# Kernel tuning notes

Hardware: AMD Instinct MI355X
Metric: run time of the kernel (lower is better)

## Reference

```python
import jax, jax.numpy as jnp
import numpy as np

N_NODES, N_EDGES = 50000, 800000
N_IN, E_IN, N_OUT, E_OUT = 64, 32, 64, 32


def _xavier(key, fan_in, fan_out):
    std = (2.0 / (fan_in + fan_out)) ** 0.5
    return jax.random.normal(key, (fan_in, fan_out), dtype=jnp.float32) * std


def setup_inputs() -> dict:
    key = jax.random.key(0)
    ks = jax.random.split(key, 10)
    return {
        "feat": jax.random.normal(ks[0], (N_NODES, N_IN), dtype=jnp.float32),
        "edge_feat": jax.random.normal(ks[1], (N_EDGES, E_IN), dtype=jnp.float32),
        "w_msg": _xavier(ks[2], N_IN + E_IN, N_OUT),
        "b_msg": jnp.zeros((N_OUT,), dtype=jnp.float32),
        "w_node": _xavier(ks[3], N_IN + N_OUT, N_OUT),
        "b_node": jnp.zeros((N_OUT,), dtype=jnp.float32),
        "w_edge": _xavier(ks[4], N_IN + N_OUT + E_IN, E_OUT),
        "b_edge": jnp.zeros((E_OUT,), dtype=jnp.float32),
        "src_idx": jax.random.randint(ks[5], (N_EDGES,), 0, N_NODES, dtype=jnp.int32),
        "dst_idx": jax.random.randint(ks[6], (N_EDGES,), 0, N_NODES, dtype=jnp.int32),
    }


def reference(feat, edge_feat, w_msg, b_msg, w_node, b_node, w_edge, b_edge, src_idx, dst_idx):
    n_nodes = feat.shape[0]
    # --- message: gather src + edge, linear, tanh --- [E, n_out]
    src_h = feat[src_idx]
    m = jnp.tanh(jnp.concatenate([src_h, edge_feat], axis=1) @ w_msg + b_msg)
    # --- scatter-mean into destination nodes --- [N, n_out]
    sums = jax.ops.segment_sum(m, dst_idx, num_segments=n_nodes)
    cnt = jax.ops.segment_sum(jnp.ones((m.shape[0], 1), m.dtype), dst_idx, num_segments=n_nodes)
    neigh = sums / jnp.maximum(cnt, 1.0)
    # --- node update: cat([neigh, h]) -> linear -> tanh (dropout = identity in eval) ---
    h = jnp.tanh(jnp.concatenate([neigh, feat], axis=1) @ w_node + b_node)
    # --- edge update: cat([src h, dst neigh(updated), edge h]) -> linear -> tanh ---
    e = jnp.tanh(jnp.concatenate([src_h, h[dst_idx], edge_feat], axis=1) @ w_edge + b_edge)
    return h, e
```

## Files before the change

kernel.cpp:

```cpp
#include <hip/hip_runtime.h>

#define NNODES 50000
#define NEDGES 800000
#define NPAD   50176
#define NTILE_E (NEDGES / 16)
#define NTILE_N (NNODES / 16)

typedef __attribute__((ext_vector_type(8))) short bf16x8;
typedef __attribute__((ext_vector_type(4))) float f32x4;

union ABu { bf16x8 v; uint4 u; };

__device__ __forceinline__ float fast_tanh(float x) {
    float e = __expf(2.0f * x);
    return 1.0f - 2.0f * __builtin_amdgcn_rcpf(e + 1.0f);
}

__device__ __forceinline__ unsigned pk_rne(float x, float y) {
    unsigned a = __float_as_uint(x), b = __float_as_uint(y);
    a = (a + 0x7fffu + ((a >> 16) & 1u)) >> 16;
    b = (b + 0x7fffu + ((b >> 16) & 1u)) >> 16;
    return a | (b << 16);
}
__device__ __forceinline__ unsigned pk_tr(float a, float b) {
    return __builtin_amdgcn_perm(__float_as_uint(b), __float_as_uint(a), 0x07060302);
}
__device__ __forceinline__ float bf16_lo(unsigned u) { return __uint_as_float(u << 16); }
__device__ __forceinline__ float bf16_hi(unsigned u) { return __uint_as_float(u & 0xffff0000u); }

__device__ __forceinline__ ABu make_afrag(const float* p) {
    float4 a = ((const float4*)p)[0];
    float4 b = ((const float4*)p)[1];
    ABu r;
    r.u.x = pk_tr(a.x, a.y); r.u.y = pk_tr(a.z, a.w);
    r.u.z = pk_tr(b.x, b.y); r.u.w = pk_tr(b.z, b.w);
    return r;
}

template <int LDW>
__device__ __forceinline__ ABu make_bfrag(const float* wp) {
    ABu r;
    r.u.x = pk_rne(wp[0 * LDW], wp[1 * LDW]);
    r.u.y = pk_rne(wp[2 * LDW], wp[3 * LDW]);
    r.u.z = pk_rne(wp[4 * LDW], wp[5 * LDW]);
    r.u.w = pk_rne(wp[6 * LDW], wp[7 * LDW]);
    return r;
}

#define MFMA(a, b, c) __builtin_amdgcn_mfma_f32_16x16x32_bf16((a).v, (b).v, (c), 0, 0, 0)

__global__ __launch_bounds__(256) void hist_kernel(const int* __restrict__ dst_idx,
                                                   int* __restrict__ cnt) {
    const int t = blockIdx.x * 256 + threadIdx.x;
    const int base = t * 4;
    if (base + 4 <= NEDGES) {
        int4 d = *(const int4*)(dst_idx + base);
        atomicAdd(&cnt[d.x], 1);
        atomicAdd(&cnt[d.y], 1);
        atomicAdd(&cnt[d.z], 1);
        atomicAdd(&cnt[d.w], 1);
    } else {
        for (int i = base; i < NEDGES; ++i) atomicAdd(&cnt[dst_idx[i]], 1);
    }
}

__global__ __launch_bounds__(256) void msg_kernel(
    const float* __restrict__ feat, const float* __restrict__ edge_feat,
    const float* __restrict__ w_msg, const float* __restrict__ b_msg,
    const int* __restrict__ src_idx, const int* __restrict__ dst_idx,
    unsigned* __restrict__ m_out, int* __restrict__ off) {
    __shared__ __align__(16) float wl[96 * 64];
    for (int i = threadIdx.x; i < 96 * 64; i += 256) wl[i] = w_msg[i];
    __syncthreads();

    const int lane = threadIdx.x & 63, wave = threadIdx.x >> 6;
    const int col = lane & 15, quad = lane >> 4;

    ABu bf[3][4];
#pragma unroll
    for (int kc = 0; kc < 3; ++kc)
#pragma unroll
        for (int nt = 0; nt < 4; ++nt)
            bf[kc][nt] = make_bfrag<64>(&wl[(kc * 32 + quad * 8) * 64 + nt * 16 + col]);

    float bias[4];
#pragma unroll
    for (int nt = 0; nt < 4; ++nt) bias[nt] = b_msg[nt * 16 + col];

    const int nw = gridDim.x << 2;
    for (int t = (blockIdx.x << 2) + wave; t < NTILE_E; t += nw) {
        const int e0 = t << 4;
        const int e = e0 + col;
        const int src = src_idx[e];
        int pos = 0;
        if (quad == 0) pos = atomicAdd(&off[dst_idx[e]], 1);

        ABu a0 = make_afrag(feat + (size_t)src * 64 + quad * 8);
        ABu a1 = make_afrag(feat + (size_t)src * 64 + 32 + quad * 8);
        ABu a2 = make_afrag(edge_feat + (size_t)e * 32 + quad * 8);

        f32x4 acc[4];
#pragma unroll
        for (int nt = 0; nt < 4; ++nt)
            acc[nt] = (f32x4){bias[nt], bias[nt], bias[nt], bias[nt]};
#pragma unroll
        for (int nt = 0; nt < 4; ++nt) {
            acc[nt] = MFMA(a0, bf[0][nt], acc[nt]);
            acc[nt] = MFMA(a1, bf[1][nt], acc[nt]);
            acc[nt] = MFMA(a2, bf[2][nt], acc[nt]);
        }
#pragma unroll
        for (int i = 0; i < 4; ++i) {
            const int row = __shfl(pos, (quad << 2) + i);
            uint2 o;
            o.x = pk_rne(fast_tanh(acc[0][i]), fast_tanh(acc[1][i]));
            o.y = pk_rne(fast_tanh(acc[2][i]), fast_tanh(acc[3][i]));
            *(uint2*)(m_out + (size_t)row * 32 + (col << 1)) = o;
        }
    }
}

__global__ __launch_bounds__(256) void scan1(const int* __restrict__ cnt,
                                             int* __restrict__ off,
                                             int* __restrict__ btot) {
    __shared__ int s[256];
    const int tid = threadIdx.x;
    const int g = blockIdx.x * 256 + tid;
    const int own = cnt[g];
    s[tid] = own;
    __syncthreads();
    for (int o = 1; o < 256; o <<= 1) {
        int v = (tid >= o) ? s[tid - o] : 0;
        __syncthreads();
        s[tid] += v;
        __syncthreads();
    }
    off[g] = s[tid] - own;
    if (tid == 255) btot[blockIdx.x] = s[255];
}

__global__ __launch_bounds__(256) void scan2(int* __restrict__ btot) {
    __shared__ int s[256];
    const int tid = threadIdx.x;
    const int own = btot[tid];
    s[tid] = own;
    __syncthreads();
    for (int o = 1; o < 256; o <<= 1) {
        int v = (tid >= o) ? s[tid - o] : 0;
        __syncthreads();
        s[tid] += v;
        __syncthreads();
    }
    btot[tid] = s[tid] - own;
}

__global__ __launch_bounds__(256) void scan3(int* __restrict__ off,
                                             const int* __restrict__ btot) {
    const int g = blockIdx.x * 256 + threadIdx.x;
    off[g] += btot[blockIdx.x];
}

__global__ __launch_bounds__(256) void gather_kernel(
    const unsigned* __restrict__ m,
    const int* __restrict__ off , const int* __restrict__ cnt,
    float* __restrict__ neigh) {
    const int wave = threadIdx.x >> 6;
    const int lane = threadIdx.x & 63;
    const int n = blockIdx.x * 4 + wave;
    if (n >= NNODES) return;
    const int c = cnt[n];
    const int o = off[n] - c;
    const int q = lane & 15;
    const int g = lane >> 4;

    float a0 = 0.f, a1 = 0.f, a2 = 0.f, a3 = 0.f;
    for (int r = g; r < c; r += 4) {
        const uint2 u = *(const uint2*)(m + (size_t)(o + r) * 32 + (q << 1));
        a0 += bf16_lo(u.x);
        a1 += bf16_hi(u.x);
        a2 += bf16_lo(u.y);
        a3 += bf16_hi(u.y);
    }
    a0 += __shfl_xor(a0, 16); a1 += __shfl_xor(a1, 16);
    a2 += __shfl_xor(a2, 16); a3 += __shfl_xor(a3, 16);
    a0 += __shfl_xor(a0, 32); a1 += __shfl_xor(a1, 32);
    a2 += __shfl_xor(a2, 32); a3 += __shfl_xor(a3, 32);
    if (g == 0) {
        const float inv = __builtin_amdgcn_rcpf((float)max(c, 1));
        float4 o4 = {a0 * inv, a1 * inv, a2 * inv, a3 * inv};
        ((float4*)(neigh + (size_t)n * 64))[q] = o4;
    }
}

__device__ __forceinline__ int mapk(int ks) {
    return ks < 64 ? ((ks >> 2) + ((ks >> 1) & 1) * 32 + (ks & 1) * 16) : ks;
}

__global__ __launch_bounds__(256) void node_update(
    const float* __restrict__ feat,
    const float* __restrict__ w_node, const float* __restrict__ b_node,
    float* __restrict__ h) {
    __shared__ __align__(16) float wl[128 * 64];
    for (int i = threadIdx.x; i < 128 * 64; i += 256) wl[i] = w_node[i];
    __syncthreads();

    const int lane = threadIdx.x & 63, wave = threadIdx.x >> 6;
    const int col = lane & 15, quad = lane >> 4;

    ABu bf[4][4];
#pragma unroll
    for (int kc = 0; kc < 4; ++kc)
#pragma unroll
        for (int nt = 0; nt < 4; ++nt) {
            unsigned p[4];
#pragma unroll
            for (int jj = 0; jj < 4; ++jj) {
                const int k0 = kc * 32 + quad * 8 + jj * 2;
                p[jj] = pk_rne(wl[mapk(k0) * 64 + nt * 16 + col],
                               wl[mapk(k0 + 1) * 64 + nt * 16 + col]);
            }
            bf[kc][nt].u = (uint4){p[0], p[1], p[2], p[3]};
        }

    float bias[4];
#pragma unroll
    for (int nt = 0; nt < 4; ++nt) bias[nt] = b_node[nt * 16 + col];

    const int nw = gridDim.x << 2;
    for (int t = (blockIdx.x << 2) + wave; t < NTILE_N; t += nw) {
        const int n0 = t << 4;
        const int n = n0 + col;
        ABu a0 = make_afrag(h + (size_t)n * 64 + quad * 8);
        ABu a1 = make_afrag(h + (size_t)n * 64 + 32 + quad * 8);
        ABu a2 = make_afrag(feat + (size_t)n * 64 + quad * 8);
        ABu a3 = make_afrag(feat + (size_t)n * 64 + 32 + quad * 8);

        f32x4 acc[4];
#pragma unroll
        for (int nt = 0; nt < 4; ++nt)
            acc[nt] = (f32x4){bias[nt], bias[nt], bias[nt], bias[nt]};
#pragma unroll
        for (int nt = 0; nt < 4; ++nt) {
            acc[nt] = MFMA(a0, bf[0][nt], acc[nt]);
            acc[nt] = MFMA(a1, bf[1][nt], acc[nt]);
            acc[nt] = MFMA(a2, bf[2][nt], acc[nt]);
            acc[nt] = MFMA(a3, bf[3][nt], acc[nt]);
        }
#pragma unroll
        for (int i = 0; i < 4; ++i) {
            const int nr = n0 + quad * 4 + i;
#pragma unroll
            for (int nt = 0; nt < 4; ++nt)
                h[(size_t)nr * 64 + nt * 16 + col] = fast_tanh(acc[nt][i]);
        }
    }
}

__global__ __launch_bounds__(256) void edge_update(
    const float* __restrict__ feat, const float* __restrict__ edge_feat,
    const float* __restrict__ h,
    const float* __restrict__ w_edge, const float* __restrict__ b_edge,
    const int* __restrict__ src_idx, const int* __restrict__ dst_idx,
    float* __restrict__ e_out) {
    __shared__ __align__(16) float wl[160 * 32];
    for (int i = threadIdx.x; i < 160 * 32; i += 256) wl[i] = w_edge[i];
    __syncthreads();

    const int lane = threadIdx.x & 63, wave = threadIdx.x >> 6;
    const int col = lane & 15, quad = lane >> 4;

    ABu bf[5][2];
#pragma unroll
    for (int kc = 0; kc < 5; ++kc)
#pragma unroll
        for (int nt = 0; nt < 2; ++nt)
            bf[kc][nt] = make_bfrag<32>(&wl[(kc * 32 + quad * 8) * 32 + nt * 16 + col]);

    float bias[2];
#pragma unroll
    for (int nt = 0; nt < 2; ++nt) bias[nt] = b_edge[nt * 16 + col];

    const int nw = gridDim.x << 2;
    for (int t = (blockIdx.x << 2) + wave; t < NTILE_E; t += nw) {
        const int e0 = t << 4;
        const int e = e0 + col;
        const int src = src_idx[e];
        const int dst = dst_idx[e];

        ABu a0 = make_afrag(feat + (size_t)src * 64 + quad * 8);
        ABu a1 = make_afrag(feat + (size_t)src * 64 + 32 + quad * 8);
        ABu a2 = make_afrag(h + (size_t)dst * 64 + quad * 8);
        ABu a3 = make_afrag(h + (size_t)dst * 64 + 32 + quad * 8);
        ABu a4 = make_afrag(edge_feat + (size_t)e * 32 + quad * 8);

        f32x4 acc[2];
#pragma unroll
        for (int nt = 0; nt < 2; ++nt)
            acc[nt] = (f32x4){bias[nt], bias[nt], bias[nt], bias[nt]};
#pragma unroll
        for (int nt = 0; nt < 2; ++nt) {
            acc[nt] = MFMA(a0, bf[0][nt], acc[nt]);
            acc[nt] = MFMA(a1, bf[1][nt], acc[nt]);
            acc[nt] = MFMA(a2, bf[2][nt], acc[nt]);
            acc[nt] = MFMA(a3, bf[3][nt], acc[nt]);
            acc[nt] = MFMA(a4, bf[4][nt], acc[nt]);
        }
#pragma unroll
        for (int i = 0; i < 4; ++i) {
            const int er = e0 + quad * 4 + i;
            e_out[(size_t)er * 32 + col] = fast_tanh(acc[0][i]);
            e_out[(size_t)er * 32 + 16 + col] = fast_tanh(acc[1][i]);
        }
    }
}

extern "C" void kernel_launch(void* const* d_in, const int* in_sizes, int n_in,
                              void* d_out, int out_size, void* d_ws, size_t ws_size,
                              hipStream_t stream) {
    const float* feat      = (const float*)d_in[0];
    const float* edge_feat = (const float*)d_in[1];
    const float* w_msg     = (const float*)d_in[2];
    const float* b_msg     = (const float*)d_in[3];
    const float* w_node    = (const float*)d_in[4];
    const float* b_node    = (const float*)d_in[5];
    const float* w_edge    = (const float*)d_in[6];
    const float* b_edge    = (const float*)d_in[7];
    const int*   src_idx   = (const int*)d_in[8];
    const int*   dst_idx   = (const int*)d_in[9];

    float* h = (float*)d_out;
    float* e = (float*)d_out + (size_t)NNODES * 64;
    unsigned* m = (unsigned*)e;

    int* cnt  = (int*)d_ws;
    int* off  = cnt + NPAD;
    int* btot = off + NPAD;

    hipMemsetAsync(cnt, 0, NPAD * sizeof(int), stream);
    hipMemsetAsync(btot, 0, 256 * sizeof(int), stream);

    hist_kernel<<<(NEDGES / 4 + 255) / 256, 256, 0, stream>>>(dst_idx, cnt);
    scan1<<<NPAD / 256, 256, 0, stream>>>(cnt, off, btot);
    scan2<<<1, 256, 0, stream>>>(btot);
    scan3<<<NPAD / 256, 256, 0, stream>>>(off, btot);
    msg_kernel<<<1536, 256, 0, stream>>>(feat, edge_feat, w_msg, b_msg,
                                         src_idx, dst_idx, m, off);
    gather_kernel<<<NNODES / 4, 256, 0, stream>>>(m, off, cnt, h);
    node_update<<<512, 256, 0, stream>>>(feat, w_node, b_node, h);
    edge_update<<<2048, 256, 0, stream>>>(feat, edge_feat, h, w_edge,
                                          b_edge, src_idx, dst_idx, e);
}
```

Measured before the change: 430.1 us.

## Precompute edge ranks in histogram, double-buffer loads in message and edge kernels

The histogram kernel now records each edge's rank within its destination bucket, so the message kernel computes output rows as off+rank and no longer needs atomics on the offset array. The message and edge-update kernels gain a two-slot software pipeline that issues the next tile's gathers before computing the current tile. Weights are staged into shared memory already packed as bf16 pairs, and the gather kernel uses 16-byte loads with 8 rows in flight per wave. This adds a rank workspace array, raises register pressure from the double buffers, and lowers the edge-update grid size.

```diff
diff --git a/kernel.cpp b/kernel.cpp
--- a/kernel.cpp
+++ b/kernel.cpp
@@ -37,86 +37,38 @@
     return r;
 }
 
-template <int LDW>
-__device__ __forceinline__ ABu make_bfrag(const float* wp) {
+template <int LDN>
+__device__ __forceinline__ ABu make_bfrag_u(const unsigned* wp) {
     ABu r;
-    r.u.x = pk_rne(wp[0 * LDW], wp[1 * LDW]);
-    r.u.y = pk_rne(wp[2 * LDW], wp[3 * LDW]);
-    r.u.z = pk_rne(wp[4 * LDW], wp[5 * LDW]);
-    r.u.w = pk_rne(wp[6 * LDW], wp[7 * LDW]);
+    r.u.x = wp[0 * LDN]; r.u.y = wp[1 * LDN];
+    r.u.z = wp[2 * LDN]; r.u.w = wp[3 * LDN];
     return r;
 }
 
+template <int KH, int N>
+__device__ __forceinline__ void stage_w(const float* __restrict__ w, unsigned* wl_u) {
+    for (int i = threadIdx.x; i < KH * N; i += 256) {
+        const int kp = i / N, n = i % N;
+        wl_u[i] = pk_rne(w[(2 * kp) * N + n], w[(2 * kp + 1) * N + n]);
+    }
+}
+
 #define MFMA(a, b, c) __builtin_amdgcn_mfma_f32_16x16x32_bf16((a).v, (b).v, (c), 0, 0, 0)
 
 __global__ __launch_bounds__(256) void hist_kernel(const int* __restrict__ dst_idx,
-                                                   int* __restrict__ cnt) {
-    const int t = blockIdx.x * 256 + threadIdx.x;
-    const int base = t * 4;
+                                                   int* __restrict__ cnt,
+                                                   int* __restrict__ rank) {
+    const int base = (blockIdx.x * 256 + threadIdx.x) * 4;
     if (base + 4 <= NEDGES) {
         int4 d = *(const int4*)(dst_idx + base);
-        atomicAdd(&cnt[d.x], 1);
-        atomicAdd(&cnt[d.y], 1);
-        atomicAdd(&cnt[d.z], 1);
-        atomicAdd(&cnt[d.w], 1);
+        int4 r;
+        r.x = atomicAdd(&cnt[d.x], 1);
+        r.y = atomicAdd(&cnt[d.y], 1);
+        r.z = atomicAdd(&cnt[d.z], 1);
+        r.w = atomicAdd(&cnt[d.w], 1);
+        *(int4*)(rank + base) = r;
     } else {
-        for (int i = base; i < NEDGES; ++i) atomicAdd(&cnt[dst_idx[i]], 1);
-    }
-}
-
-__global__ __launch_bounds__(256) void msg_kernel(
-    const float* __restrict__ feat, const float* __restrict__ edge_feat,
-    const float* __restrict__ w_msg, const float* __restrict__ b_msg,
-    const int* __restrict__ src_idx, const int* __restrict__ dst_idx,
-    unsigned* __restrict__ m_out, int* __restrict__ off) {
-    __shared__ __align__(16) float wl[96 * 64];
-    for (int i = threadIdx.x; i < 96 * 64; i += 256) wl[i] = w_msg[i];
-    __syncthreads();
-
-    const int lane = threadIdx.x & 63, wave = threadIdx.x >> 6;
-    const int col = lane & 15, quad = lane >> 4;
-
-    ABu bf[3][4];
-#pragma unroll
-    for (int kc = 0; kc < 3; ++kc)
-#pragma unroll
-        for (int nt = 0; nt < 4; ++nt)
-            bf[kc][nt] = make_bfrag<64>(&wl[(kc * 32 + quad * 8) * 64 + nt * 16 + col]);
-
-    float bias[4];
-#pragma unroll
-    for (int nt = 0; nt < 4; ++nt) bias[nt] = b_msg[nt * 16 + col];
-
-    const int nw = gridDim.x << 2;
-    for (int t = (blockIdx.x << 2) + wave; t < NTILE_E; t += nw) {
-        const int e0 = t << 4;
-        const int e = e0 + col;
-        const int src = src_idx[e];
-        int pos = 0;
-        if (quad == 0) pos = atomicAdd(&off[dst_idx[e]], 1);
-
-        ABu a0 = make_afrag(feat + (size_t)src * 64 + quad * 8);
-        ABu a1 = make_afrag(feat + (size_t)src * 64 + 32 + quad * 8);
-        ABu a2 = make_afrag(edge_feat + (size_t)e * 32 + quad * 8);
-
-        f32x4 acc[4];
-#pragma unroll
-        for (int nt = 0; nt < 4; ++nt)
-            acc[nt] = (f32x4){bias[nt], bias[nt], bias[nt], bias[nt]};
-#pragma unroll
-        for (int nt = 0; nt < 4; ++nt) {
-            acc[nt] = MFMA(a0, bf[0][nt], acc[nt]);
-            acc[nt] = MFMA(a1, bf[1][nt], acc[nt]);
-            acc[nt] = MFMA(a2, bf[2][nt], acc[nt]);
-        }
-#pragma unroll
-        for (int i = 0; i < 4; ++i) {
-            const int row = __shfl(pos, (quad << 2) + i);
-            uint2 o;
-            o.x = pk_rne(fast_tanh(acc[0][i]), fast_tanh(acc[1][i]));
-            o.y = pk_rne(fast_tanh(acc[2][i]), fast_tanh(acc[3][i]));
-            *(uint2*)(m_out + (size_t)row * 32 + (col << 1)) = o;
-        }
+        for (int i = base; i < NEDGES; ++i) rank[i] = atomicAdd(&cnt[dst_idx[i]], 1);
     }
 }
 
@@ -160,6 +112,94 @@
     off[g] += btot[blockIdx.x];
 }
 
+struct MsgBuf { ABu a0, a1, a2; int4 rows; };
+
+__device__ __forceinline__ void msg_load(
+    int t, int col, int quad,
+    const float* __restrict__ feat, const float* __restrict__ edge_feat,
+    const int* __restrict__ src_idx, const int* __restrict__ dst_idx,
+    const int* __restrict__ off, const int* __restrict__ rank, MsgBuf& b) {
+    const int e0 = t << 4;
+    const int e = e0 + col;
+    const int src = src_idx[e];
+    const int4 d4 = *(const int4*)(dst_idx + e0 + (quad << 2));
+    const int4 r4 = *(const int4*)(rank + e0 + (quad << 2));
+    b.rows.x = off[d4.x] + r4.x;
+    b.rows.y = off[d4.y] + r4.y;
+    b.rows.z = off[d4.z] + r4.z;
+    b.rows.w = off[d4.w] + r4.w;
+    b.a0 = make_afrag(feat + (size_t)src * 64 + (quad << 3));
+    b.a1 = make_afrag(feat + (size_t)src * 64 + 32 + (quad << 3));
+    b.a2 = make_afrag(edge_feat + (size_t)e * 32 + (quad << 3));
+}
+
+__device__ __forceinline__ void msg_comp(
+    int col, const ABu (&bf)[3][4], const float (&bias)[4],
+    const MsgBuf& b, unsigned* __restrict__ m_out) {
+    f32x4 acc[4];
+#pragma unroll
+    for (int nt = 0; nt < 4; ++nt)
+        acc[nt] = (f32x4){bias[nt], bias[nt], bias[nt], bias[nt]};
+#pragma unroll
+    for (int nt = 0; nt < 4; ++nt) {
+        acc[nt] = MFMA(b.a0, bf[0][nt], acc[nt]);
+        acc[nt] = MFMA(b.a1, bf[1][nt], acc[nt]);
+        acc[nt] = MFMA(b.a2, bf[2][nt], acc[nt]);
+    }
+    const int rw[4] = {b.rows.x, b.rows.y, b.rows.z, b.rows.w};
+#pragma unroll
+    for (int i = 0; i < 4; ++i) {
+        uint2 o;
+        o.x = pk_rne(fast_tanh(acc[0][i]), fast_tanh(acc[1][i]));
+        o.y = pk_rne(fast_tanh(acc[2][i]), fast_tanh(acc[3][i]));
+        *(uint2*)(m_out + (size_t)rw[i] * 32 + (col << 1)) = o;
+    }
+}
+
+__global__ __launch_bounds__(256) void msg_kernel(
+    const float* __restrict__ feat, const float* __restrict__ edge_feat,
+    const float* __restrict__ w_msg, const float* __restrict__ b_msg,
+    const int* __restrict__ src_idx, const int* __restrict__ dst_idx,
+    const int* __restrict__ off, const int* __restrict__ rank,
+    unsigned* __restrict__ m_out) {
+    __shared__ __align__(16) unsigned wl[48 * 64];
+    stage_w<48, 64>(w_msg, wl);
+    __syncthreads();
+
+    const int lane = threadIdx.x & 63, wave = threadIdx.x >> 6;
+    const int col = lane & 15, quad = lane >> 4;
+
+    ABu bf[3][4];
+#pragma unroll
+    for (int kc = 0; kc < 3; ++kc)
+#pragma unroll
+        for (int nt = 0; nt < 4; ++nt)
+            bf[kc][nt] = make_bfrag_u<64>(&wl[(kc * 16 + (quad << 2)) * 64 + nt * 16 + col]);
+
+    float bias[4];
+#pragma unroll
+    for (int nt = 0; nt < 4; ++nt) bias[nt] = b_msg[nt * 16 + col];
+
+    const int nw = gridDim.x << 2;
+    int t = (blockIdx.x << 2) + wave;
+    if (t >= NTILE_E) return;
+    MsgBuf A, B;
+    msg_load(t, col, quad, feat, edge_feat, src_idx, dst_idx, off, rank, A);
+    for (;;) {
+        const int t2 = t + nw;
+        if (t2 < NTILE_E)
+            msg_load(t2, col, quad, feat, edge_feat, src_idx, dst_idx, off, rank, B);
+        msg_comp(col, bf, bias, A, m_out);
+        if (t2 >= NTILE_E) return;
+        const int t3 = t2 + nw;
+        if (t3 < NTILE_E)
+            msg_load(t3, col, quad, feat, edge_feat, src_idx, dst_idx, off, rank, A);
+        msg_comp(col, bf, bias, B, m_out);
+        if (t3 >= NTILE_E) return;
+        t = t3;
+    }
+}
+
 __global__ __launch_bounds__(256) void gather_kernel(
     const unsigned* __restrict__ m,
     const int* __restrict__ off , const int* __restrict__ cnt,
@@ -169,26 +209,33 @@
     const int n = blockIdx.x * 4 + wave;
     if (n >= NNODES) return;
     const int c = cnt[n];
-    const int o = off[n] - c;
-    const int q = lane & 15;
-    const int g = lane >> 4;
-
-    float a0 = 0.f, a1 = 0.f, a2 = 0.f, a3 = 0.f;
-    for (int r = g; r < c; r += 4) {
-        const uint2 u = *(const uint2*)(m + (size_t)(o + r) * 32 + (q << 1));
-        a0 += bf16_lo(u.x);
-        a1 += bf16_hi(u.x);
-        a2 += bf16_lo(u.y);
-        a3 += bf16_hi(u.y);
-    }
-    a0 += __shfl_xor(a0, 16); a1 += __shfl_xor(a1, 16);
-    a2 += __shfl_xor(a2, 16); a3 += __shfl_xor(a3, 16);
-    a0 += __shfl_xor(a0, 32); a1 += __shfl_xor(a1, 32);
-    a2 += __shfl_xor(a2, 32); a3 += __shfl_xor(a3, 32);
+    const int o = off[n];
+    const int q = lane & 7;
+    const int g = lane >> 3;
+
+    float s[8];
+#pragma unroll
+    for (int j = 0; j < 8; ++j) s[j] = 0.f;
+    for (int r = g; r < c; r += 8) {
+        const uint4 u = *(const uint4*)(m + (size_t)(o + r) * 32 + (q << 2));
+        s[0] += bf16_lo(u.x); s[1] += bf16_hi(u.x);
+        s[2] += bf16_lo(u.y); s[3] += bf16_hi(u.y);
+        s[4] += bf16_lo(u.z); s[5] += bf16_hi(u.z);
+        s[6] += bf16_lo(u.w); s[7] += bf16_hi(u.w);
+    }
+#pragma unroll
+    for (int j = 0; j < 8; ++j) {
+        s[j] += __shfl_xor(s[j], 8);
+        s[j] += __shfl_xor(s[j], 16);
+        s[j] += __shfl_xor(s[j], 32);
+    }
     if (g == 0) {
         const float inv = __builtin_amdgcn_rcpf((float)max(c, 1));
-        float4 o4 = {a0 * inv, a1 * inv, a2 * inv, a3 * inv};
-        ((float4*)(neigh + (size_t)n * 64))[q] = o4;
+        float4 o0 = {s[0] * inv, s[1] * inv, s[2] * inv, s[3] * inv};
+        float4 o1 = {s[4] * inv, s[5] * inv, s[6] * inv, s[7] * inv};
+        float* dst = neigh + (size_t)n * 64 + (q << 3);
+        ((float4*)dst)[0] = o0;
+        ((float4*)dst)[1] = o1;
     }
 }
 
@@ -256,14 +303,55 @@
     }
 }
 
+struct EBuf { ABu a0, a1, a2, a3, a4; };
+
+__device__ __forceinline__ void edge_load(
+    int t, int col, int quad,
+    const float* __restrict__ feat, const float* __restrict__ edge_feat,
+    const float* __restrict__ h,
+    const int* __restrict__ src_idx, const int* __restrict__ dst_idx, EBuf& b) {
+    const int e = (t << 4) + col;
+    const int src = src_idx[e];
+    const int dst = dst_idx[e];
+    b.a0 = make_afrag(feat + (size_t)src * 64 + (quad << 3));
+    b.a1 = make_afrag(feat + (size_t)src * 64 + 32 + (quad << 3));
+    b.a2 = make_afrag(h + (size_t)dst * 64 + (quad << 3));
+    b.a3 = make_afrag(h + (size_t)dst * 64 + 32 + (quad << 3));
+    b.a4 = make_afrag(edge_feat + (size_t)e * 32 + (quad << 3));
+}
+
+__device__ __forceinline__ void edge_comp(
+    int t, int col, int quad, const ABu (&bf)[5][2], const float (&bias)[2],
+    const EBuf& b, float* __restrict__ e_out) {
+    f32x4 acc[2];
+#pragma unroll
+    for (int nt = 0; nt < 2; ++nt)
+        acc[nt] = (f32x4){bias[nt], bias[nt], bias[nt], bias[nt]};
+#pragma unroll
+    for (int nt = 0; nt < 2; ++nt) {
+        acc[nt] = MFMA(b.a0, bf[0][nt], acc[nt]);
+        acc[nt] = MFMA(b.a1, bf[1][nt], acc[nt]);
+        acc[nt] = MFMA(b.a2, bf[2][nt], acc[nt]);
+        acc[nt] = MFMA(b.a3, bf[3][nt], acc[nt]);
+        acc[nt] = MFMA(b.a4, bf[4][nt], acc[nt]);
+    }
+    const int e0 = t << 4;
+#pragma unroll
+    for (int i = 0; i < 4; ++i) {
+        const int er = e0 + quad * 4 + i;
+        e_out[(size_t)er * 32 + col] = fast_tanh(acc[0][i]);
+        e_out[(size_t)er * 32 + 16 + col] = fast_tanh(acc[1][i]);
+    }
+}
+
 __global__ __launch_bounds__(256) void edge_update(
     const float* __restrict__ feat, const float* __restrict__ edge_feat,
     const float* __restrict__ h,
     const float* __restrict__ w_edge, const float* __restrict__ b_edge,
     const int* __restrict__ src_idx, const int* __restrict__ dst_idx,
     float* __restrict__ e_out) {
-    __shared__ __align__(16) float wl[160 * 32];
-    for (int i = threadIdx.x; i < 160 * 32; i += 256) wl[i] = w_edge[i];
+    __shared__ __align__(16) unsigned wl[80 * 32];
+    stage_w<80, 32>(w_edge, wl);
     __syncthreads();
 
     const int lane = threadIdx.x & 63, wave = threadIdx.x >> 6;
@@ -274,43 +362,29 @@
     for (int kc = 0; kc < 5; ++kc)
 #pragma unroll
         for (int nt = 0; nt < 2; ++nt)
-            bf[kc][nt] = make_bfrag<32>(&wl[(kc * 32 + quad * 8) * 32 + nt * 16 + col]);
+            bf[kc][nt] = make_bfrag_u<32>(&wl[(kc * 16 + (quad << 2)) * 32 + nt * 16 + col]);
 
     float bias[2];
 #pragma unroll
     for (int nt = 0; nt < 2; ++nt) bias[nt] = b_edge[nt * 16 + col];
 
     const int nw = gridDim.x << 2;
-    for (int t = (blockIdx.x << 2) + wave; t < NTILE_E; t += nw) {
-        const int e0 = t << 4;
-        const int e = e0 + col;
-        const int src = src_idx[e];
-        const int dst = dst_idx[e];
-
-        ABu a0 = make_afrag(feat + (size_t)src * 64 + quad * 8);
-        ABu a1 = make_afrag(feat + (size_t)src * 64 + 32 + quad * 8);
-        ABu a2 = make_afrag(h + (size_t)dst * 64 + quad * 8);
-        ABu a3 = make_afrag(h + (size_t)dst * 64 + 32 + quad * 8);
-        ABu a4 = make_afrag(edge_feat + (size_t)e * 32 + quad * 8);
-
-        f32x4 acc[2];
-#pragma unroll
-        for (int nt = 0; nt < 2; ++nt)
-            acc[nt] = (f32x4){bias[nt], bias[nt], bias[nt], bias[nt]};
-#pragma unroll
-        for (int nt = 0; nt < 2; ++nt) {
-            acc[nt] = MFMA(a0, bf[0][nt], acc[nt]);
-            acc[nt] = MFMA(a1, bf[1][nt], acc[nt]);
-            acc[nt] = MFMA(a2, bf[2][nt], acc[nt]);
-            acc[nt] = MFMA(a3, bf[3][nt], acc[nt]);
-            acc[nt] = MFMA(a4, bf[4][nt], acc[nt]);
-        }
-#pragma unroll
-        for (int i = 0; i < 4; ++i) {
-            const int er = e0 + quad * 4 + i;
-            e_out[(size_t)er * 32 + col] = fast_tanh(acc[0][i]);
-            e_out[(size_t)er * 32 + 16 + col] = fast_tanh(acc[1][i]);
-        }
+    int t = (blockIdx.x << 2) + wave;
+    if (t >= NTILE_E) return;
+    EBuf A, B;
+    edge_load(t, col, quad, feat, edge_feat, h, src_idx, dst_idx, A);
+    for (;;) {
+        const int t2 = t + nw;
+        if (t2 < NTILE_E)
+            edge_load(t2, col, quad, feat, edge_feat, h, src_idx, dst_idx, B);
+        edge_comp(t, col, quad, bf, bias, A, e_out);
+        if (t2 >= NTILE_E) return;
+        const int t3 = t2 + nw;
+        if (t3 < NTILE_E)
+            edge_load(t3, col, quad, feat, edge_feat, h, src_idx, dst_idx, A);
+        edge_comp(t2, col, quad, bf, bias, B, e_out);
+        if (t3 >= NTILE_E) return;
+        t = t3;
     }
 }
 
@@ -335,18 +409,19 @@
     int* cnt  = (int*)d_ws;
     int* off  = cnt + NPAD;
     int* btot = off + NPAD;
+    int* rank = btot + 256;
 
     hipMemsetAsync(cnt, 0, NPAD * sizeof(int), stream);
     hipMemsetAsync(btot, 0, 256 * sizeof(int), stream);
 
-    hist_kernel<<<(NEDGES / 4 + 255) / 256, 256, 0, stream>>>(dst_idx, cnt);
+    hist_kernel<<<(NEDGES / 4 + 255) / 256, 256, 0, stream>>>(dst_idx, cnt, rank);
     scan1<<<NPAD / 256, 256, 0, stream>>>(cnt, off, btot);
     scan2<<<1, 256, 0, stream>>>(btot);
     scan3<<<NPAD / 256, 256, 0, stream>>>(off, btot);
     msg_kernel<<<1536, 256, 0, stream>>>(feat, edge_feat, w_msg, b_msg,
-                                         src_idx, dst_idx, m, off);
+                                         src_idx, dst_idx, off, rank, m);
     gather_kernel<<<NNODES / 4, 256, 0, stream>>>(m, off, cnt, h);
     node_update<<<512, 256, 0, stream>>>(feat, w_node, b_node, h);
-    edge_update<<<2048, 256, 0, stream>>>(feat, edge_feat, h, w_edge,
+    edge_update<<<1280, 256, 0, stream>>>(feat, edge_feat, h, w_edge,
                                           b_edge, src_idx, dst_idx, e);
 }
```

After: 414.6 us. 3.6% less time.
